# Performance work log

Measured on AMD Instinct MI355X. Metric: run time of the kernel, lower is better.

The kernel has to match this reference:

```python
import jax, jax.numpy as jnp
import numpy as np
from math import sqrt

B, N, D = 16, 4096, 128
M = 64 * 24  # mem_size_per_joint * num_joints


def setup_inputs() -> dict:
    key = jax.random.key(0)
    kx, km = jax.random.split(key)
    x = jax.random.normal(kx, (B, N, D), dtype=jnp.float32)
    mem = jax.random.normal(km, (1, D, M), dtype=jnp.float32)  # N(0,1) init as in torch
    return {"x": x, "mem": mem}


def reference(x, mem):
    # x: (B, N, D); mem: (1, D, M)
    d = x.shape[-1]
    w = mem[0]  # (D, M)
    # logits = bmm(m_key (B,M,D), x_ (B,D,N)) / sqrt(D)  -> (B, M, N)
    logits = jnp.einsum('dm,bnd->bmn', w, x) / sqrt(d)
    # softmax over the memory axis (dim=1 in torch layout)
    attn = jax.nn.softmax(logits, axis=1)  # (B, M, N)
    # x_new = bmm(m (B,D,M), attn) -> (B,D,N); output permuted to (B,N,D)
    out = jnp.einsum('dm,bmn->bnd', w, attn)
    return out
```

## Files before the change

### kernel.cpp

```cpp
#include <hip/hip_runtime.h>
#include <math.h>


#define Bdim 16
#define Ndim 4096
#define Ddim 128
#define Mdim 1536
#define NT 64
#define NTHREADS 256
#define NSESS 12
#define SESS_M 128
#define XPAD 136
#define PPAD 136
#define NFRAG 24576

typedef __attribute__((ext_vector_type(8))) _Float16 f16x8;
typedef __attribute__((ext_vector_type(4))) _Float16 f16x4;
typedef __attribute__((ext_vector_type(4))) float    f32x4;

__global__ void jamb_prep(const float* __restrict__ w,
                          _Float16* __restrict__ wt,
                          _Float16* __restrict__ wd) {
    const int tid = blockIdx.x * 256 + threadIdx.x;
    const float SC = 0.08838834764831843f;
    if (tid < NFRAG) {
        const int f    = tid;
        const int lane = f & 63;
        const int fs   = f >> 6;
        const int ks   = fs & 3;
        const int mt   = fs >> 2;
        const int m    = mt * 16 + (lane & 15);
        const int d0   = ks * 32 + (lane >> 4) * 8;
        f16x8 pk;
        #pragma unroll
        for (int j = 0; j < 8; ++j)
            pk[j] = (_Float16)(w[(size_t)(d0 + j) * Mdim + m] * SC);
        *(f16x8*)&wt[(size_t)f * 8] = pk;
    } else {
        const int f    = tid - NFRAG;
        const int lane = f & 63;
        const int fs   = f >> 6;
        const int km   = fs % 48;
        const int dt   = fs / 48;
        const int d    = dt * 16 + (lane & 15);
        const int m0   = km * 32 + (lane >> 4) * 8;
        const float* src = w + (size_t)d * Mdim + m0;
        const float4 v0 = *(const float4*)src;
        const float4 v1 = *(const float4*)(src + 4);
        f16x8 pk;
        pk[0] = (_Float16)v0.x; pk[1] = (_Float16)v0.y;
        pk[2] = (_Float16)v0.z; pk[3] = (_Float16)v0.w;
        pk[4] = (_Float16)v1.x; pk[5] = (_Float16)v1.y;
        pk[6] = (_Float16)v1.z; pk[7] = (_Float16)v1.w;
        *(f16x8*)&wd[(size_t)f * 8] = pk;
    }
}

__global__ __launch_bounds__(NTHREADS, 4)
void jamb_mfma_kernel(const float* __restrict__ x,
                      const _Float16* __restrict__ wt,
                      const _Float16* __restrict__ wd,
                      float* __restrict__ out) {
    __shared__ __align__(16) _Float16 xs[NT * XPAD];
    __shared__ __align__(16) _Float16 Pbuf[NT * PPAD];
    __shared__ float redsum[4][4][16];

    const int t    = threadIdx.x;
    const int w    = t >> 6;
    const int l    = t & 63;
    const int c16  = l & 15;
    const int quad = l >> 4;

    const int blk   = blockIdx.x;
    const int b     = blk >> 6;
    const int nbase = (blk & 63) * NT;

    {
        const float* xb = x + (size_t)(b * Ndim + nbase) * Ddim;
        #pragma unroll
        for (int i = 0; i < 8; ++i) {
            const int f   = t + i * 256;
            const int row = f >> 5;
            const int c4  = (f & 31) * 4;
            const float4 v = *(const float4*)(xb + row * Ddim + c4);
            f16x4 pk;
            pk[0] = (_Float16)v.x; pk[1] = (_Float16)v.y;
            pk[2] = (_Float16)v.z; pk[3] = (_Float16)v.w;
            *(f16x4*)&xs[row * XPAD + c4] = pk;
        }
    }
    __syncthreads();

    const f16x8* WT = (const f16x8*)wt;
    const f16x8* WD = (const f16x8*)wd;

    float sums[4] = {0.f, 0.f, 0.f, 0.f};
    f32x4 c[2][4];
    #pragma unroll
    for (int i = 0; i < 2; ++i)
        #pragma unroll
        for (int nt = 0; nt < 4; ++nt) c[i][nt] = (f32x4){0.f, 0.f, 0.f, 0.f};

    f32x4 acc[2][4];

    auto p1mfma = [&](int q) {
        const int mtb = q * 8 + w * 2;
        #pragma unroll
        for (int i = 0; i < 2; ++i)
            #pragma unroll
            for (int nt = 0; nt < 4; ++nt) acc[i][nt] = (f32x4){0.f, 0.f, 0.f, 0.f};
        #pragma unroll
        for (int s = 0; s < 4; ++s) {
            const f16x8 fh0 = WT[((mtb + 0) * 4 + s) * 64 + l];
            const f16x8 fh1 = WT[((mtb + 1) * 4 + s) * 64 + l];
            f16x8 bx[4];
            #pragma unroll
            for (int nt = 0; nt < 4; ++nt)
                bx[nt] = *(const f16x8*)&xs[(nt * 16 + c16) * XPAD + s * 32 + quad * 8];
            #pragma unroll
            for (int nt = 0; nt < 4; ++nt) {
                acc[0][nt] = __builtin_amdgcn_mfma_f32_16x16x32_f16(fh0, bx[nt], acc[0][nt], 0, 0, 0);
                acc[1][nt] = __builtin_amdgcn_mfma_f32_16x16x32_f16(fh1, bx[nt], acc[1][nt], 0, 0, 0);
            }
        }
    };

    auto expwrite = [&]() {
        #pragma unroll
        for (int i = 0; i < 2; ++i) {
            const int mloc = (w * 2 + i) * 16 + quad * 4;
            #pragma unroll
            for (int nt = 0; nt < 4; ++nt) {
                const float e0 = __expf(acc[i][nt][0]);
                const float e1 = __expf(acc[i][nt][1]);
                const float e2 = __expf(acc[i][nt][2]);
                const float e3 = __expf(acc[i][nt][3]);
                sums[nt] += (e0 + e1) + (e2 + e3);
                f16x4 pk;
                pk[0] = (_Float16)e0; pk[1] = (_Float16)e1;
                pk[2] = (_Float16)e2; pk[3] = (_Float16)e3;
                *(f16x4*)&Pbuf[(nt * 16 + c16) * PPAD + mloc] = pk;
            }
        }
    };

    auto p2 = [&](int q) {
        #pragma unroll
        for (int sk = 0; sk < 4; ++sk) {
            const f16x8 a0 = WD[((2 * w)     * 48 + q * 4 + sk) * 64 + l];
            const f16x8 a1 = WD[((2 * w + 1) * 48 + q * 4 + sk) * 64 + l];
            f16x8 p[4];
            #pragma unroll
            for (int nt = 0; nt < 4; ++nt)
                p[nt] = *(const f16x8*)&Pbuf[(nt * 16 + c16) * PPAD + sk * 32 + quad * 8];
            #pragma unroll
            for (int nt = 0; nt < 4; ++nt) {
                c[0][nt] = __builtin_amdgcn_mfma_f32_16x16x32_f16(a0, p[nt], c[0][nt], 0, 0, 0);
                c[1][nt] = __builtin_amdgcn_mfma_f32_16x16x32_f16(a1, p[nt], c[1][nt], 0, 0, 0);
            }
        }
    };

    p1mfma(0);
    expwrite();
    #pragma unroll 1
    for (int q = 0; q < NSESS; ++q) {
        __syncthreads();
        p2(q);
        if (q + 1 < NSESS) p1mfma(q + 1);
        __syncthreads();
        if (q + 1 < NSESS) expwrite();
    }

    #pragma unroll
    for (int nt = 0; nt < 4; ++nt) {
        sums[nt] += __shfl_xor(sums[nt], 16, 64);
        sums[nt] += __shfl_xor(sums[nt], 32, 64);
    }
    if (quad == 0) {
        #pragma unroll
        for (int nt = 0; nt < 4; ++nt) redsum[w][nt][c16] = sums[nt];
    }
    __syncthreads();

    float inv[4];
    #pragma unroll
    for (int nt = 0; nt < 4; ++nt)
        inv[nt] = 1.f / ((redsum[0][nt][c16] + redsum[1][nt][c16]) +
                         (redsum[2][nt][c16] + redsum[3][nt][c16]));

    #pragma unroll
    for (int dt2 = 0; dt2 < 2; ++dt2) {
        #pragma unroll
        for (int nt = 0; nt < 4; ++nt) {
            float* op = out + (size_t)(b * Ndim + nbase + nt * 16 + c16) * Ddim
                           + (2 * w + dt2) * 16 + quad * 4;
            float4 o;
            o.x = c[dt2][nt][0] * inv[nt];
            o.y = c[dt2][nt][1] * inv[nt];
            o.z = c[dt2][nt][2] * inv[nt];
            o.w = c[dt2][nt][3] * inv[nt];
            *(float4*)op = o;
        }
    }
}

extern "C" void kernel_launch(void* const* d_in, const int* in_sizes, int n_in,
                              void* d_out, int out_size, void* d_ws, size_t ws_size,
                              hipStream_t stream) {
    const float* x = (const float*)d_in[0];
    const float* w = (const float*)d_in[1];
    float* out = (float*)d_out;
    (void)in_sizes; (void)n_in; (void)out_size; (void)ws_size;

    _Float16* wt = (_Float16*)d_ws;
    _Float16* wd = wt + Ddim * Mdim;

    jamb_prep<<<dim3((2 * NFRAG) / 256), dim3(256), 0, stream>>>(w, wt, wd);
    jamb_mfma_kernel<<<dim3((Bdim * Ndim) / NT), dim3(NTHREADS), 0, stream>>>(x, wt, wd, out);
}
```

Baseline: 138.7 us.

## Switch fused attention GEMMs to 32x32x16 MFMA with 2x2 wave tiling

Both GEMMs move from 16x16x32 MFMA tiles to 32x32x16 tiles, with waves arranged as a 2x2 grid over M/D and N instead of each wave covering all 64 rows. This cuts the LDS fragment reads per MFMA and the number of instructions issued, and simplifies the softmax row-sum reduction. The weight-prep kernel is rewritten to stage tiles through shared memory for coalesced transposition into the new fragment layouts. In exchange, per-wave global weight loads change pattern and each wave reads more distinct weight fragments, which could add L2 traffic.

```diff
diff --git a/kernel.cpp b/kernel.cpp
--- a/kernel.cpp
+++ b/kernel.cpp
@@ -9,50 +9,54 @@
 #define NT 64
 #define NTHREADS 256
 #define NSESS 12
-#define SESS_M 128
 #define XPAD 136
 #define PPAD 136
-#define NFRAG 24576
-
-typedef __attribute__((ext_vector_type(8))) _Float16 f16x8;
-typedef __attribute__((ext_vector_type(4))) _Float16 f16x4;
-typedef __attribute__((ext_vector_type(4))) float    f32x4;
-
-__global__ void jamb_prep(const float* __restrict__ w,
-                          _Float16* __restrict__ wt,
-                          _Float16* __restrict__ wd) {
-    const int tid = blockIdx.x * 256 + threadIdx.x;
+
+typedef __attribute__((ext_vector_type(8)))  _Float16 f16x8;
+typedef __attribute__((ext_vector_type(4)))  _Float16 f16x4;
+typedef __attribute__((ext_vector_type(16))) float    f32x16;
+
+__global__ __launch_bounds__(256)
+void jamb_prep(const float* __restrict__ w,
+               _Float16* __restrict__ wt,
+               _Float16* __restrict__ wd) {
+    __shared__ float ts[32 * 132];
+    const int t  = threadIdx.x;
+    const int mt = blockIdx.x;
+    #pragma unroll
+    for (int i = 0; i < 16; ++i) {
+        const int f = t + i * 256;
+        const int d = f >> 5;
+        const int m = f & 31;
+        ts[m * 132 + d] = w[(size_t)d * Mdim + mt * 32 + m];
+    }
+    __syncthreads();
     const float SC = 0.08838834764831843f;
-    if (tid < NFRAG) {
-        const int f    = tid;
-        const int lane = f & 63;
-        const int fs   = f >> 6;
-        const int ks   = fs & 3;
-        const int mt   = fs >> 2;
-        const int m    = mt * 16 + (lane & 15);
-        const int d0   = ks * 32 + (lane >> 4) * 8;
+    #pragma unroll
+    for (int h = 0; h < 2; ++h) {
+        const int fr = t + h * 256;
+        const int l  = fr & 63;
+        const int ks = fr >> 6;
+        const int m  = l & 31;
+        const int d0 = ks * 16 + (l >> 5) * 8;
         f16x8 pk;
         #pragma unroll
         for (int j = 0; j < 8; ++j)
-            pk[j] = (_Float16)(w[(size_t)(d0 + j) * Mdim + m] * SC);
-        *(f16x8*)&wt[(size_t)f * 8] = pk;
-    } else {
-        const int f    = tid - NFRAG;
-        const int lane = f & 63;
-        const int fs   = f >> 6;
-        const int km   = fs % 48;
-        const int dt   = fs / 48;
-        const int d    = dt * 16 + (lane & 15);
-        const int m0   = km * 32 + (lane >> 4) * 8;
-        const float* src = w + (size_t)d * Mdim + m0;
-        const float4 v0 = *(const float4*)src;
-        const float4 v1 = *(const float4*)(src + 4);
+            pk[j] = (_Float16)(ts[m * 132 + d0 + j] * SC);
+        *(f16x8*)&wt[(size_t)((mt * 8 + ks) * 64 + l) * 8] = pk;
+    }
+    #pragma unroll
+    for (int h = 0; h < 2; ++h) {
+        const int l    = t & 63;
+        const int dt   = t >> 6;
+        const int km   = mt * 2 + h;
+        const int d    = dt * 32 + (l & 31);
+        const int mloc = h * 16 + (l >> 5) * 8;
         f16x8 pk;
-        pk[0] = (_Float16)v0.x; pk[1] = (_Float16)v0.y;
-        pk[2] = (_Float16)v0.z; pk[3] = (_Float16)v0.w;
-        pk[4] = (_Float16)v1.x; pk[5] = (_Float16)v1.y;
-        pk[6] = (_Float16)v1.z; pk[7] = (_Float16)v1.w;
-        *(f16x8*)&wd[(size_t)f * 8] = pk;
+        #pragma unroll
+        for (int j = 0; j < 8; ++j)
+            pk[j] = (_Float16)ts[(mloc + j) * 132 + d];
+        *(f16x8*)&wd[(size_t)((km * 4 + dt) * 64 + l) * 8] = pk;
     }
 }
 
@@ -63,13 +67,15 @@
                       float* __restrict__ out) {
     __shared__ __align__(16) _Float16 xs[NT * XPAD];
     __shared__ __align__(16) _Float16 Pbuf[NT * PPAD];
-    __shared__ float redsum[4][4][16];
-
-    const int t    = threadIdx.x;
-    const int w    = t >> 6;
-    const int l    = t & 63;
-    const int c16  = l & 15;
-    const int quad = l >> 4;
+    __shared__ float redsum[2][2][32];
+
+    const int t   = threadIdx.x;
+    const int w   = t >> 6;
+    const int l   = t & 63;
+    const int l31 = l & 31;
+    const int hi  = l >> 5;
+    const int wm2 = w >> 1;
+    const int wn2 = w & 1;
 
     const int blk   = blockIdx.x;
     const int b     = blk >> 6;
@@ -94,70 +100,56 @@
     const f16x8* WT = (const f16x8*)wt;
     const f16x8* WD = (const f16x8*)wd;
 
-    float sums[4] = {0.f, 0.f, 0.f, 0.f};
-    f32x4 c[2][4];
-    #pragma unroll
-    for (int i = 0; i < 2; ++i)
-        #pragma unroll
-        for (int nt = 0; nt < 4; ++nt) c[i][nt] = (f32x4){0.f, 0.f, 0.f, 0.f};
-
-    f32x4 acc[2][4];
+    const int nrow = wn2 * 32 + l31;
+
+    float ssum = 0.f;
+    f32x16 c[2];
+    c[0] = (f32x16)(0.f);
+    c[1] = (f32x16)(0.f);
+    f32x16 acc[2];
 
     auto p1mfma = [&](int q) {
-        const int mtb = q * 8 + w * 2;
-        #pragma unroll
-        for (int i = 0; i < 2; ++i)
+        const int mtb = q * 4 + 2 * wm2;
+        acc[0] = (f32x16)(0.f);
+        acc[1] = (f32x16)(0.f);
+        #pragma unroll
+        for (int ks = 0; ks < 8; ++ks) {
+            const f16x8 fh0 = WT[(size_t)((mtb + 0) * 8 + ks) * 64 + l];
+            const f16x8 fh1 = WT[(size_t)((mtb + 1) * 8 + ks) * 64 + l];
+            const f16x8 bx  = *(const f16x8*)&xs[nrow * XPAD + ks * 16 + hi * 8];
+            acc[0] = __builtin_amdgcn_mfma_f32_32x32x16_f16(fh0, bx, acc[0], 0, 0, 0);
+            acc[1] = __builtin_amdgcn_mfma_f32_32x32x16_f16(fh1, bx, acc[1], 0, 0, 0);
+        }
+    };
+
+    auto expwrite = [&]() {
+        #pragma unroll
+        for (int i = 0; i < 2; ++i) {
+            const int mbase = (2 * wm2 + i) * 32;
             #pragma unroll
-            for (int nt = 0; nt < 4; ++nt) acc[i][nt] = (f32x4){0.f, 0.f, 0.f, 0.f};
-        #pragma unroll
-        for (int s = 0; s < 4; ++s) {
-            const f16x8 fh0 = WT[((mtb + 0) * 4 + s) * 64 + l];
-            const f16x8 fh1 = WT[((mtb + 1) * 4 + s) * 64 + l];
-            f16x8 bx[4];
-            #pragma unroll
-            for (int nt = 0; nt < 4; ++nt)
-                bx[nt] = *(const f16x8*)&xs[(nt * 16 + c16) * XPAD + s * 32 + quad * 8];
-            #pragma unroll
-            for (int nt = 0; nt < 4; ++nt) {
-                acc[0][nt] = __builtin_amdgcn_mfma_f32_16x16x32_f16(fh0, bx[nt], acc[0][nt], 0, 0, 0);
-                acc[1][nt] = __builtin_amdgcn_mfma_f32_16x16x32_f16(fh1, bx[nt], acc[1][nt], 0, 0, 0);
-            }
-        }
-    };
-
-    auto expwrite = [&]() {
-        #pragma unroll
-        for (int i = 0; i < 2; ++i) {
-            const int mloc = (w * 2 + i) * 16 + quad * 4;
-            #pragma unroll
-            for (int nt = 0; nt < 4; ++nt) {
-                const float e0 = __expf(acc[i][nt][0]);
-                const float e1 = __expf(acc[i][nt][1]);
-                const float e2 = __expf(acc[i][nt][2]);
-                const float e3 = __expf(acc[i][nt][3]);
-                sums[nt] += (e0 + e1) + (e2 + e3);
+            for (int g = 0; g < 4; ++g) {
+                const float e0 = __expf(acc[i][4 * g + 0]);
+                const float e1 = __expf(acc[i][4 * g + 1]);
+                const float e2 = __expf(acc[i][4 * g + 2]);
+                const float e3 = __expf(acc[i][4 * g + 3]);
+                ssum += (e0 + e1) + (e2 + e3);
                 f16x4 pk;
                 pk[0] = (_Float16)e0; pk[1] = (_Float16)e1;
                 pk[2] = (_Float16)e2; pk[3] = (_Float16)e3;
-                *(f16x4*)&Pbuf[(nt * 16 + c16) * PPAD + mloc] = pk;
+                *(f16x4*)&Pbuf[nrow * PPAD + mbase + g * 8 + hi * 4] = pk;
             }
         }
     };
 
     auto p2 = [&](int q) {
         #pragma unroll
-        for (int sk = 0; sk < 4; ++sk) {
-            const f16x8 a0 = WD[((2 * w)     * 48 + q * 4 + sk) * 64 + l];
-            const f16x8 a1 = WD[((2 * w + 1) * 48 + q * 4 + sk) * 64 + l];
-            f16x8 p[4];
-            #pragma unroll
-            for (int nt = 0; nt < 4; ++nt)
-                p[nt] = *(const f16x8*)&Pbuf[(nt * 16 + c16) * PPAD + sk * 32 + quad * 8];
-            #pragma unroll
-            for (int nt = 0; nt < 4; ++nt) {
-                c[0][nt] = __builtin_amdgcn_mfma_f32_16x16x32_f16(a0, p[nt], c[0][nt], 0, 0, 0);
-                c[1][nt] = __builtin_amdgcn_mfma_f32_16x16x32_f16(a1, p[nt], c[1][nt], 0, 0, 0);
-            }
+        for (int sk = 0; sk < 8; ++sk) {
+            const int km = q * 8 + sk;
+            const f16x8 a0 = WD[(size_t)(km * 4 + 2 * wm2 + 0) * 64 + l];
+            const f16x8 a1 = WD[(size_t)(km * 4 + 2 * wm2 + 1) * 64 + l];
+            const f16x8 pf = *(const f16x8*)&Pbuf[nrow * PPAD + sk * 16 + hi * 8];
+            c[0] = __builtin_amdgcn_mfma_f32_32x32x16_f16(a0, pf, c[0], 0, 0, 0);
+            c[1] = __builtin_amdgcn_mfma_f32_32x32x16_f16(a1, pf, c[1], 0, 0, 0);
         }
     };
 
@@ -172,35 +164,23 @@
         if (q + 1 < NSESS) expwrite();
     }
 
-    #pragma unroll
-    for (int nt = 0; nt < 4; ++nt) {
-        sums[nt] += __shfl_xor(sums[nt], 16, 64);
-        sums[nt] += __shfl_xor(sums[nt], 32, 64);
-    }
-    if (quad == 0) {
-        #pragma unroll
-        for (int nt = 0; nt < 4; ++nt) redsum[w][nt][c16] = sums[nt];
-    }
+    ssum += __shfl_xor(ssum, 32, 64);
+    if (hi == 0) redsum[wn2][wm2][l31] = ssum;
     __syncthreads();
-
-    float inv[4];
-    #pragma unroll
-    for (int nt = 0; nt < 4; ++nt)
-        inv[nt] = 1.f / ((redsum[0][nt][c16] + redsum[1][nt][c16]) +
-                         (redsum[2][nt][c16] + redsum[3][nt][c16]));
-
-    #pragma unroll
-    for (int dt2 = 0; dt2 < 2; ++dt2) {
-        #pragma unroll
-        for (int nt = 0; nt < 4; ++nt) {
-            float* op = out + (size_t)(b * Ndim + nbase + nt * 16 + c16) * Ddim
-                           + (2 * w + dt2) * 16 + quad * 4;
+    const float inv = 1.f / (redsum[wn2][0][l31] + redsum[wn2][1][l31]);
+
+    #pragma unroll
+    for (int i2 = 0; i2 < 2; ++i2) {
+        float* ob = out + (size_t)(b * Ndim + nbase + nrow) * Ddim
+                        + (2 * wm2 + i2) * 32;
+        #pragma unroll
+        for (int g = 0; g < 4; ++g) {
             float4 o;
-            o.x = c[dt2][nt][0] * inv[nt];
-            o.y = c[dt2][nt][1] * inv[nt];
-            o.z = c[dt2][nt][2] * inv[nt];
-            o.w = c[dt2][nt][3] * inv[nt];
-            *(float4*)op = o;
+            o.x = c[i2][4 * g + 0] * inv;
+            o.y = c[i2][4 * g + 1] * inv;
+            o.z = c[i2][4 * g + 2] * inv;
+            o.w = c[i2][4 * g + 3] * inv;
+            *(float4*)(ob + g * 8 + hi * 4) = o;
         }
     }
 }
@@ -216,6 +196,6 @@
     _Float16* wt = (_Float16*)d_ws;
     _Float16* wd = wt + Ddim * Mdim;
 
-    jamb_prep<<<dim3((2 * NFRAG) / 256), dim3(256), 0, stream>>>(w, wt, wd);
+    jamb_prep<<<dim3(48), dim3(256), 0, stream>>>(w, wt, wd);
     jamb_mfma_kernel<<<dim3((Bdim * Ndim) / NT), dim3(NTHREADS), 0, stream>>>(x, wt, wd, out);
 }
```

Result: slower. 145.4 us (+4.8%).
